# Optimization experiments

Hardware: AMD Instinct MI355X
Metric: run time of the kernel (lower is better)

Reference implementation:

```python
import jax, jax.numpy as jnp
import numpy as np

N = 100000      # nodes
E = 1600000     # edges (avg degree 16)
F_IN = 64       # num_features
HID = 16        # hidden channels (fixed in module)
OUT = 32        # num_classes
K = 2           # kernel_size (dim=1, degree=1 open B-spline -> 2 basis fns)


def setup_inputs() -> dict:
    key = jax.random.key(0)
    ks = jax.random.split(key, 8)
    return {
        "x": jax.random.normal(ks[0], (N, F_IN), jnp.float32),
        "edge_index": jax.random.randint(ks[1], (2, E), 0, N, dtype=jnp.int64),
        "dropout": 0,  # unused in eval mode (F.dropout training=False)
        "edge_attr": jnp.full((E, 1), 0.1, jnp.float32),  # nt([0.1]) broadcast per edge
        "W1": jax.random.normal(ks[2], (K, F_IN, HID), jnp.float32) / np.sqrt(K * F_IN).astype(np.float32),
        "root1": jax.random.normal(ks[3], (F_IN, HID), jnp.float32) / np.sqrt(F_IN).astype(np.float32),
        "bias1": jnp.zeros((HID,), jnp.float32),
        "W2": jax.random.normal(ks[4], (K, HID, OUT), jnp.float32) / np.sqrt(K * HID).astype(np.float32),
        "root2": jax.random.normal(ks[5], (HID, OUT), jnp.float32) / np.sqrt(HID).astype(np.float32),
        "bias2": jnp.zeros((OUT,), jnp.float32),
    }


def spline_conv(x, edge_index, edge_attr, W, root, bias):
    """SplineConv, dim=1, kernel_size=2, degree=1 open B-spline, aggr='mean'."""
    src, dst = edge_index[0], edge_index[1]
    n = x.shape[0]
    u = edge_attr[:, 0]                                  # [E] pseudo-coords in [0,1]
    # degree-1 open spline, kernel_size=2: frac = u*(ks-1) = u; kernels {0,1}
    basis = jnp.stack([1.0 - u, u], axis=1)              # [E, K]
    # transform at node level (cheaper than gathering raw features per edge)
    h = jnp.einsum('nf,kfo->nko', x, W)                  # [N, K, out]
    msg = jnp.einsum('ek,eko->eo', basis, h[src])        # [E, out]
    summed = jax.ops.segment_sum(msg, dst, num_segments=n)
    deg = jax.ops.segment_sum(jnp.ones_like(u), dst, num_segments=n)
    out = summed / jnp.maximum(deg, 1.0)[:, None]        # mean aggregation
    return out + x @ root + bias                          # root weight + bias


def reference(x, edge_index, dropout, edge_attr, W1, root1, bias1, W2, root2, bias2):
    # dropout is a no-op in eval mode
    h = jax.nn.elu(spline_conv(x, edge_index, edge_attr, W1, root1, bias1))
    h = spline_conv(h, edge_index, edge_attr, W2, root2, bias2)
    return jax.nn.log_softmax(h, axis=1)
```

## Files before the change

kernel.cpp:

```cpp
#include <hip/hip_runtime.h>
#include <math.h>

#define NN 100000
#define NE 1600000
#define F_IN 64
#define HID 16
#define OUTF 32
#define BKT_SHIFT 6
#define BKT_NODES 64
#define NBKT 1563
#define SRCM 0x1FFFF
#define CAP_REG 2048
#define CAP_LDS 1184
#define PBLK3 200
#define EPB3 8000
#define CHUNK 2000
#define NCHK 4
#define OVF_MAX 4096

__device__ __forceinline__ unsigned bf16r(float f) {
    unsigned u = __float_as_uint(f);
    return (u + 0x7FFFu + ((u >> 16) & 1u)) >> 16;
}
__device__ __forceinline__ float bfa(unsigned p) { return __uint_as_float(p << 16); }
__device__ __forceinline__ float bfd(unsigned p) { return __uint_as_float(p & 0xFFFF0000u); }
__device__ __forceinline__ float bfh(unsigned short v) { return __uint_as_float(((unsigned)v) << 16); }

__device__ __forceinline__ void acc8(uint4 hv, float u, float* s0, float* s1) {
    unsigned w[4] = {hv.x, hv.y, hv.z, hv.w};
#pragma unroll
    for (int q = 0; q < 4; ++q) {
        float lo = __uint_as_float(w[q] << 16);
        float hi = __uint_as_float(w[q] & 0xFFFF0000u);
        s0[2 * q]     += lo; s1[2 * q]     = fmaf(u, lo, s1[2 * q]);
        s0[2 * q + 1] += hi; s1[2 * q + 1] = fmaf(u, hi, s1[2 * q + 1]);
    }
}
__device__ __forceinline__ void acc4(uint4 ap, float u, float* a) {
    unsigned w[4] = {ap.x, ap.y, ap.z, ap.w};
#pragma unroll
    for (int q = 0; q < 4; ++q)
        a[q] += fmaf(u, bfd(w[q]), bfa(w[q]));
}

__global__ __launch_bounds__(1024) void partF_kernel(const int* __restrict__ ei,
                                                     const float* __restrict__ ea,
                                                     int* __restrict__ gcur,
                                                     int* __restrict__ novf,
                                                     int4* __restrict__ ovf,
                                                     int2* __restrict__ bkt) {
    __shared__ int gpos[NBKT];
    __shared__ int segc[NBKT];
    __shared__ int pw[16];
    __shared__ int2 sbuf[CHUNK];
    int t = threadIdx.x, blk = blockIdx.x;
    for (int i = t; i < NBKT; i += 1024) gpos[i] = 0;
    __syncthreads();
    int beg = blk * EPB3;
    for (int i = t; i < EPB3 / 4; i += 1024) {
        int4 d4 = *(const int4*)(ei + NE + beg + 4 * i);
        atomicAdd(&gpos[d4.x >> BKT_SHIFT], 1);
        atomicAdd(&gpos[d4.y >> BKT_SHIFT], 1);
        atomicAdd(&gpos[d4.z >> BKT_SHIFT], 1);
        atomicAdd(&gpos[d4.w >> BKT_SHIFT], 1);
    }
    __syncthreads();
    int rot = (blk * 397) % NBKT;
    for (int k = t; k < NBKT; k += 1024) {
        int i = k + rot; if (i >= NBKT) i -= NBKT;
        int c = gpos[i];
        gpos[i] = c ? atomicAdd(&gcur[i], c) : 0;
    }
    __syncthreads();
    for (int c = 0; c < NCHK; ++c) {
        int cbeg = beg + c * CHUNK;
        for (int i = t; i < NBKT; i += 1024) segc[i] = 0;
        __syncthreads();
        for (int i = t; i < CHUNK / 4; i += 1024) {
            int4 d4 = *(const int4*)(ei + NE + cbeg + 4 * i);
            atomicAdd(&segc[d4.x >> BKT_SHIFT], 1);
            atomicAdd(&segc[d4.y >> BKT_SHIFT], 1);
            atomicAdd(&segc[d4.z >> BKT_SHIFT], 1);
            atomicAdd(&segc[d4.w >> BKT_SHIFT], 1);
        }
        __syncthreads();
        int i0 = 2 * t, i1 = 2 * t + 1;
        int v0 = (i0 < NBKT) ? segc[i0] : 0;
        int v1 = (i1 < NBKT) ? segc[i1] : 0;
        int ts = v0 + v1;
        int lane = t & 63, wid = t >> 6;
        int sc = ts;
#pragma unroll
        for (int off = 1; off < 64; off <<= 1) {
            int o = __shfl_up(sc, off, 64);
            if (lane >= off) sc += o;
        }
        if (lane == 63) pw[wid] = sc;
        __syncthreads();
        if (t < 16) {
            int p = pw[t];
            int q = p;
#pragma unroll
            for (int off = 1; off < 16; off <<= 1) {
                int o = __shfl_up(q, off, 64);
                if (t >= off) q += o;
            }
            pw[t] = q - p;
        }
        __syncthreads();
        int ebase = pw[wid] + (sc - ts);
        if (i0 < NBKT) segc[i0] = ebase;
        if (i1 < NBKT) segc[i1] = ebase + v0;
        __syncthreads();
        for (int i = t; i < CHUNK / 4; i += 1024) {
            int4 d4 = *(const int4*)(ei + NE + cbeg + 4 * i);
            int4 s4 = *(const int4*)(ei + cbeg + 4 * i);
            float4 u4 = *(const float4*)(ea + cbeg + 4 * i);
            int dst[4] = {d4.x, d4.y, d4.z, d4.w};
            int src[4] = {s4.x, s4.y, s4.z, s4.w};
            float uu[4] = {u4.x, u4.y, u4.z, u4.w};
#pragma unroll
            for (int k = 0; k < 4; ++k) {
                int b = dst[k] >> BKT_SHIFT;
                int pos = atomicAdd(&segc[b], 1);
                sbuf[pos] = make_int2(src[k] | ((dst[k] & (BKT_NODES - 1)) << 17),
                                      __float_as_int(uu[k]));
            }
        }
        __syncthreads();
        for (int i = t; i < CHUNK; i += 1024) {
            int lo = 0, hi = NBKT - 1;
            while (lo < hi) {
                int mid = (lo + hi) >> 1;
                if (segc[mid] > i) hi = mid; else lo = mid + 1;
            }
            int b = lo;
            int start = b ? segc[b - 1] : 0;
            int p = gpos[b] + (i - start);
            int2 pk = sbuf[i];
            if (p < CAP_REG) {
                bkt[(size_t)b * CAP_REG + p] = pk;
            } else {
                int o = atomicAdd(novf, 1);
                if (o < OVF_MAX)
                    ovf[o] = make_int4(b * BKT_NODES + (((unsigned)pk.x) >> 17), pk.x & SRCM, pk.y, 0);
            }
        }
        __syncthreads();
        for (int b = t; b < NBKT; b += 1024) {
            int start = b ? segc[b - 1] : 0;
            gpos[b] += segc[b] - start;
        }
        __syncthreads();
    }
}

__global__ __launch_bounds__(256) void proj1z_kernel(const float* __restrict__ x,
                                                     const float* __restrict__ W1,
                                                     const float* __restrict__ root1,
                                                     const float* __restrict__ bias1,
                                                     unsigned* __restrict__ ab1p,
                                                     float* __restrict__ r1,
                                                     int* __restrict__ gcur,
                                                     int* __restrict__ novf) {
    int gz = blockIdx.x * 256 + threadIdx.x;
    if (gz < NBKT) gcur[gz] = 0;
    if (gz == NBKT) novf[0] = 0;
    __shared__ float w[2 * F_IN * HID];
    __shared__ float wr[F_IN * HID];
    __shared__ float bb[HID];
    for (int i = threadIdx.x; i < 2 * F_IN * HID; i += 256) w[i] = W1[i];
    for (int i = threadIdx.x; i < F_IN * HID; i += 256) wr[i] = root1[i];
    if (threadIdx.x < HID) bb[threadIdx.x] = bias1[threadIdx.x];
    __syncthreads();
    int n = blockIdx.x * 256 + threadIdx.x;
    if (n >= NN) return;
    float accA[HID], accB[HID], accR[HID];
#pragma unroll
    for (int o = 0; o < HID; ++o) { accA[o] = 0.f; accB[o] = 0.f; accR[o] = bb[o]; }
    const float4* xr4 = (const float4*)(x + (size_t)n * F_IN);
    for (int f4 = 0; f4 < F_IN / 4; ++f4) {
        float4 xv4 = xr4[f4];
        float xs[4] = {xv4.x, xv4.y, xv4.z, xv4.w};
#pragma unroll
        for (int q = 0; q < 4; ++q) {
            int f = f4 * 4 + q;
            float xv = xs[q];
            const float* w0 = &w[f * HID];
            const float* w1 = &w[F_IN * HID + f * HID];
            const float* w2 = &wr[f * HID];
#pragma unroll
            for (int o = 0; o < HID; ++o) {
                accA[o] = fmaf(xv, w0[o], accA[o]);
                accB[o] = fmaf(xv, w1[o], accB[o]);
                accR[o] = fmaf(xv, w2[o], accR[o]);
            }
        }
    }
    unsigned* ar = ab1p + (size_t)n * HID;
    float* rr = r1 + (size_t)n * HID;
#pragma unroll
    for (int o = 0; o < HID; ++o) {
        ar[o] = bf16r(accA[o]) | (bf16r(accB[o] - accA[o]) << 16);
        rr[o] = accR[o];
    }
}

__global__ __launch_bounds__(256) void gather1_kernel(const int* __restrict__ gcur,
                                                      const int* __restrict__ novf,
                                                      const int4* __restrict__ ovf,
                                                      int2* __restrict__ bkt,
                                                      const unsigned* __restrict__ ab1p,
                                                      const float* __restrict__ r1,
                                                      unsigned short* __restrict__ h16,
                                                      float* __restrict__ dinv,
                                                      int* __restrict__ segg) {
    __shared__ int2 sorted[CAP_LDS];
    __shared__ int cnt[BKT_NODES], cur[BKT_NODES], segb[BKT_NODES + 1];
    __shared__ float degsL[BKT_NODES];
    int t = threadIdx.x;
    int b = blockIdx.x;
    int tot = gcur[b];
    int beg = b * CAP_REG;
    if (t < BKT_NODES) { cnt[t] = 0; cur[t] = 0; degsL[t] = 0.f; }
    __syncthreads();
    int nodeBase = b * BKT_NODES;

    if (tot <= CAP_LDS) {
        int2 myE[5];
        int nE = 0;
        for (int e = t; e < tot; e += 256) {
            int2 pk = bkt[beg + e];
            myE[nE++] = pk;
            atomicAdd(&cnt[((unsigned)pk.x) >> 17], 1);
        }
        __syncthreads();
        if (t < BKT_NODES) {
            int v = cnt[t];
            int sc = v;
#pragma unroll
            for (int off = 1; off < 64; off <<= 1) {
                int o = __shfl_up(sc, off, 64);
                if (t >= off) sc += o;
            }
            segb[t] = sc - v;
            if (t == 63) segb[64] = sc;
        }
        __syncthreads();
        for (int k = 0; k < nE; ++k) {
            int loc = ((unsigned)myE[k].x) >> 17;
            int pos = segb[loc] + atomicAdd(&cur[loc], 1);
            sorted[pos] = myE[k];
        }
        __syncthreads();
        int nv = tot >> 1;
        int4* s4 = (int4*)sorted;
        int4* o4 = (int4*)(bkt + beg);
        for (int i = t; i < nv; i += 256) o4[i] = s4[i];
        if (t == 0 && (tot & 1)) bkt[beg + tot - 1] = sorted[tot - 1];
        if (t <= BKT_NODES) segg[b * (BKT_NODES + 1) + t] = segb[t];
        int node = t >> 2;
        int jq = t & 3;
        int s0 = segb[node], e2 = segb[node + 1];
        float acc[4] = {0.f, 0.f, 0.f, 0.f};
        int e = s0;
        for (; e + 3 < e2; e += 4) {
            int2 p0 = sorted[e];
            int2 p1 = sorted[e + 1];
            int2 p2 = sorted[e + 2];
            int2 p3 = sorted[e + 3];
            uint4 a0 = *(const uint4*)(ab1p + ((size_t)(p0.x & SRCM) << 4) + (jq << 2));
            uint4 a1 = *(const uint4*)(ab1p + ((size_t)(p1.x & SRCM) << 4) + (jq << 2));
            uint4 a2 = *(const uint4*)(ab1p + ((size_t)(p2.x & SRCM) << 4) + (jq << 2));
            uint4 a3 = *(const uint4*)(ab1p + ((size_t)(p3.x & SRCM) << 4) + (jq << 2));
            acc4(a0, __int_as_float(p0.y), acc);
            acc4(a1, __int_as_float(p1.y), acc);
            acc4(a2, __int_as_float(p2.y), acc);
            acc4(a3, __int_as_float(p3.y), acc);
        }
        for (; e < e2; ++e) {
            int2 pk = sorted[e];
            uint4 ap = *(const uint4*)(ab1p + ((size_t)(pk.x & SRCM) << 4) + (jq << 2));
            acc4(ap, __int_as_float(pk.y), acc);
        }
        int n = nodeBase + node;
        if (n < NN) {
            float d0 = 1.f / (float)max(e2 - s0, 1);
            float4 rv = *(const float4*)(r1 + ((size_t)n << 4) + (jq << 2));
            float rr[4] = {rv.x, rv.y, rv.z, rv.w};
            unsigned hw[4];
#pragma unroll
            for (int k = 0; k < 4; ++k) {
                float v = acc[k] * d0 + rr[k];
                hw[k] = bf16r(v > 0.f ? v : expm1f(v));
            }
            *(uint2*)(h16 + ((size_t)n << 4) + (jq << 2)) =
                make_uint2(hw[0] | (hw[1] << 16), hw[2] | (hw[3] << 16));
            if (jq == 0) dinv[n] = d0;
        }
    } else {
        float* accL = (float*)sorted;
        int inreg = min(tot, CAP_REG);
        int end = beg + inreg;
        for (int i = t; i < BKT_NODES * HID; i += 256) accL[i] = 0.f;
        __syncthreads();
        int j = t & (HID - 1);
        int g = t >> 4;
        for (int e = beg + g; e < end; e += 16) {
            int2 pk = bkt[e];
            unsigned p = ab1p[(size_t)(pk.x & SRCM) * HID + j];
            atomicAdd(&accL[(((unsigned)pk.x) >> 17) * HID + j],
                      fmaf(__int_as_float(pk.y), bfd(p), bfa(p)));
            if (j == 0) atomicAdd(&degsL[((unsigned)pk.x) >> 17], 1.f);
        }
        int ovn = min(novf[0], OVF_MAX);
        for (int o = 0; o < ovn; ++o) {
            int4 ent = ovf[o];
            int loc = ent.x - nodeBase;
            if (loc >= 0 && loc < BKT_NODES && g == 0) {
                unsigned p = ab1p[(size_t)ent.y * HID + j];
                atomicAdd(&accL[loc * HID + j], fmaf(__int_as_float(ent.z), bfd(p), bfa(p)));
                if (j == 0) atomicAdd(&degsL[loc], 1.f);
            }
        }
        __syncthreads();
        if (t < BKT_NODES) degsL[t] = 1.f / fmaxf(degsL[t], 1.f);
        if (t == 0) segg[b * (BKT_NODES + 1)] = -1;
        __syncthreads();
        for (int idx = t; idx < BKT_NODES * HID; idx += 256) {
            int nl = idx >> 4, jj = idx & (HID - 1);
            int n = nodeBase + nl;
            if (n < NN) {
                float v = accL[idx] * degsL[nl] + r1[(size_t)n * HID + jj];
                h16[(size_t)n * HID + jj] = (unsigned short)bf16r(v > 0.f ? v : expm1f(v));
            }
        }
        if (t < BKT_NODES && nodeBase + t < NN) dinv[nodeBase + t] = degsL[t];
    }
}

#define HB_NODES 32
__global__ __launch_bounds__(256) void gather2_kernel(const int* __restrict__ gcur,
                                                      const int* __restrict__ novf,
                                                      const int4* __restrict__ ovf,
                                                      const int2* __restrict__ bkt,
                                                      const unsigned short* __restrict__ h16,
                                                      const float* __restrict__ W2,
                                                      const float* __restrict__ root2,
                                                      const float* __restrict__ bias2,
                                                      const float* __restrict__ dinv,
                                                      const int* __restrict__ segg,
                                                      float* __restrict__ out) {
    __shared__ float w20[HID * OUTF], w2d[HID * OUTF], wr[HID * OUTF];
    __shared__ float bb[OUTF];
    __shared__ int segb[HB_NODES + 1];
    __shared__ int sflag;
    int t = threadIdx.x;
    int b2 = blockIdx.x;
    int b = b2 >> 1;
    int h = b2 & 1;
    for (int i = t; i < HID * OUTF; i += 256) {
        float a = W2[i];
        w20[i] = a;
        w2d[i] = W2[HID * OUTF + i] - a;
        wr[i] = root2[i];
    }
    if (t < OUTF) bb[t] = bias2[t];
    int tot = gcur[b];
    int beg = b * CAP_REG;
    int nodeBase = b * BKT_NODES + h * HB_NODES;
    if (t <= HB_NODES) segb[t] = segg[b * (BKT_NODES + 1) + h * HB_NODES + t];
    if (t == 0) sflag = segg[b * (BKT_NODES + 1)];
    __syncthreads();

    int node = t >> 3;
    int li = t & 7;
    int sub = li >> 1;
    int jh = li & 1;
    float S0[8] = {0.f, 0.f, 0.f, 0.f, 0.f, 0.f, 0.f, 0.f};
    float S1[8] = {0.f, 0.f, 0.f, 0.f, 0.f, 0.f, 0.f, 0.f};

    if (tot <= CAP_LDS && sflag != -1) {
        const int2* sp = bkt + beg;
        int s = segb[node], e2 = segb[node + 1];
        int e = s + sub;
        for (; e + 12 < e2; e += 16) {
            int2 p0 = sp[e];
            int2 p1 = sp[e + 4];
            int2 p2 = sp[e + 8];
            int2 p3 = sp[e + 12];
            uint4 h0 = *(const uint4*)(h16 + ((size_t)(p0.x & SRCM) << 4) + (jh << 3));
            uint4 h1 = *(const uint4*)(h16 + ((size_t)(p1.x & SRCM) << 4) + (jh << 3));
            uint4 h2 = *(const uint4*)(h16 + ((size_t)(p2.x & SRCM) << 4) + (jh << 3));
            uint4 h3 = *(const uint4*)(h16 + ((size_t)(p3.x & SRCM) << 4) + (jh << 3));
            acc8(h0, __int_as_float(p0.y), S0, S1);
            acc8(h1, __int_as_float(p1.y), S0, S1);
            acc8(h2, __int_as_float(p2.y), S0, S1);
            acc8(h3, __int_as_float(p3.y), S0, S1);
        }
        for (; e < e2; e += 4) {
            int2 pk = sp[e];
            uint4 hv = *(const uint4*)(h16 + ((size_t)(pk.x & SRCM) << 4) + (jh << 3));
            acc8(hv, __int_as_float(pk.y), S0, S1);
        }
#pragma unroll
        for (int k = 0; k < 8; ++k) {
            S0[k] += __shfl_xor(S0[k], 2); S0[k] += __shfl_xor(S0[k], 4);
            S1[k] += __shfl_xor(S1[k], 2); S1[k] += __shfl_xor(S1[k], 4);
        }
    } else {
        float* s0L = w20;
        float* s1L = w2d;
        for (int i = t; i < HB_NODES * HID; i += 256) { s0L[i] = 0.f; s1L[i] = 0.f; }
        __syncthreads();
        int j = t & (HID - 1);
        int g = t >> 4;
        int inreg = min(tot, CAP_REG);
        int end = beg + inreg;
        for (int e = beg + g; e < end; e += 16) {
            int2 pk = bkt[e];
            int loc = ((unsigned)pk.x) >> 17;
            if ((loc >> 5) == h) {
                float hvv = bfh(h16[(size_t)(pk.x & SRCM) * HID + j]);
                atomicAdd(&s0L[(loc & 31) * HID + j], hvv);
                atomicAdd(&s1L[(loc & 31) * HID + j], __int_as_float(pk.y) * hvv);
            }
        }
        int ovn = min(novf[0], OVF_MAX);
        for (int o = 0; o < ovn; ++o) {
            int4 ent = ovf[o];
            int loc = ent.x - nodeBase;
            if (loc >= 0 && loc < HB_NODES && g == 0) {
                float hvv = bfh(h16[(size_t)ent.y * HID + j]);
                atomicAdd(&s0L[loc * HID + j], hvv);
                atomicAdd(&s1L[loc * HID + j], __int_as_float(ent.z) * hvv);
            }
        }
        __syncthreads();
#pragma unroll
        for (int k = 0; k < 8; ++k) {
            S0[k] = s0L[node * HID + jh * 8 + k];
            S1[k] = s1L[node * HID + jh * 8 + k];
        }
        __syncthreads();
        for (int i = t; i < HID * OUTF; i += 256) {
            float a = W2[i];
            w20[i] = a;
            w2d[i] = W2[HID * OUTF + i] - a;
        }
        __syncthreads();
    }

    float F0[16], F1[16];
#pragma unroll
    for (int k = 0; k < 8; ++k) {
        float p0 = __shfl_xor(S0[k], 1);
        float p1 = __shfl_xor(S1[k], 1);
        F0[k] = jh ? p0 : S0[k];
        F0[8 + k] = jh ? S0[k] : p0;
        F1[k] = jh ? p1 : S1[k];
        F1[8 + k] = jh ? S1[k] : p1;
    }
    int n = nodeBase + node;
    if (n < NN) {
        float di = dinv[n];
        uint4 hA = *(const uint4*)(h16 + ((size_t)n << 4));
        uint4 hB = *(const uint4*)(h16 + ((size_t)n << 4) + 8);
        float hf[16];
        unsigned wa[4] = {hA.x, hA.y, hA.z, hA.w};
        unsigned wb[4] = {hB.x, hB.y, hB.z, hB.w};
#pragma unroll
        for (int q = 0; q < 4; ++q) {
            hf[2 * q]     = __uint_as_float(wa[q] << 16);
            hf[2 * q + 1] = __uint_as_float(wa[q] & 0xFFFF0000u);
            hf[8 + 2 * q]     = __uint_as_float(wb[q] << 16);
            hf[8 + 2 * q + 1] = __uint_as_float(wb[q] & 0xFFFF0000u);
        }
        float outv[4];
#pragma unroll
        for (int q = 0; q < 4; ++q) {
            int jj = li * 4 + q;
            float ms = 0.f;
#pragma unroll
            for (int f = 0; f < HID; ++f)
                ms += F0[f] * w20[f * OUTF + jj] + F1[f] * w2d[f * OUTF + jj];
            float v = ms * di + bb[jj];
#pragma unroll
            for (int f = 0; f < HID; ++f)
                v = fmaf(hf[f], wr[f * OUTF + jj], v);
            outv[q] = v;
        }
        float m = fmaxf(fmaxf(outv[0], outv[1]), fmaxf(outv[2], outv[3]));
        m = fmaxf(m, __shfl_xor(m, 1));
        m = fmaxf(m, __shfl_xor(m, 2));
        m = fmaxf(m, __shfl_xor(m, 4));
        float sl = expf(outv[0] - m) + expf(outv[1] - m) + expf(outv[2] - m) + expf(outv[3] - m);
        sl += __shfl_xor(sl, 1);
        sl += __shfl_xor(sl, 2);
        sl += __shfl_xor(sl, 4);
        float lse = m + logf(sl);
        *(float4*)(out + (size_t)n * OUTF + li * 4) =
            make_float4(outv[0] - lse, outv[1] - lse, outv[2] - lse, outv[3] - lse);
    }
}

extern "C" void kernel_launch(void* const* d_in, const int* in_sizes, int n_in,
                              void* d_out, int out_size, void* d_ws, size_t ws_size,
                              hipStream_t stream) {
    const float* x     = (const float*)d_in[0];
    const int*   ei    = (const int*)d_in[1];
    const float* ea    = (const float*)d_in[3];
    const float* W1    = (const float*)d_in[4];
    const float* root1 = (const float*)d_in[5];
    const float* bias1 = (const float*)d_in[6];
    const float* W2    = (const float*)d_in[7];
    const float* root2 = (const float*)d_in[8];
    const float* bias2 = (const float*)d_in[9];
    float* out = (float*)d_out;
    float* ws  = (float*)d_ws;

    const size_t N = NN;
    int*            gcur = (int*)(ws);
    int*            novf = (int*)(ws + 2000);
    int4*           ovf  = (int4*)(ws + 2048);
    float*          dinv = ws + 20000;
    int*            segg = (int*)(ws + 120000);
    float*          r1   = ws + 222000;
    unsigned*       ab1p = (unsigned*)(ws + 222000 + 16 * N);
    unsigned short* h16  = (unsigned short*)(ws + 222000 + 32 * N);
    int2*           bkt  = (int2*)(ws + 222000 + 40 * N);

    int nbN = (NN + 255) / 256;
    proj1z_kernel<<<nbN, 256, 0, stream>>>(x, W1, root1, bias1, ab1p, r1, gcur, novf);
    partF_kernel<<<PBLK3, 1024, 0, stream>>>(ei, ea, gcur, novf, ovf, bkt);
    gather1_kernel<<<NBKT, 256, 0, stream>>>(gcur, novf, ovf, bkt, ab1p, r1, h16, dinv, segg);
    gather2_kernel<<<NBKT * 2, 256, 0, stream>>>(gcur, novf, ovf, bkt, h16, W2, root2, bias2, dinv, segg, out);
}
```

Baseline: 111.5 us.

## Run node projection concurrently with edge partitioning in one fused launch

```diff
diff --git a/kernel.cpp b/kernel.cpp
--- a/kernel.cpp
+++ b/kernel.cpp
@@ -17,6 +17,7 @@
 #define CHUNK 2000
 #define NCHK 4
 #define OVF_MAX 4096
+#define PROJ_BLKS 98
 
 __device__ __forceinline__ unsigned bf16r(float f) {
     unsigned u = __float_as_uint(f);
@@ -43,17 +44,73 @@
         a[q] += fmaf(u, bfd(w[q]), bfa(w[q]));
 }
 
-__global__ __launch_bounds__(1024) void partF_kernel(const int* __restrict__ ei,
-                                                     const float* __restrict__ ea,
-                                                     int* __restrict__ gcur,
-                                                     int* __restrict__ novf,
-                                                     int4* __restrict__ ovf,
-                                                     int2* __restrict__ bkt) {
+__global__ __launch_bounds__(256) void zeroG_kernel(int* __restrict__ gcur,
+                                                    int* __restrict__ novf) {
+    int t = blockIdx.x * 256 + threadIdx.x;
+    if (t < NBKT) gcur[t] = 0;
+    if (t == NBKT) novf[0] = 0;
+}
+
+__global__ __launch_bounds__(1024) void fusedPP_kernel(const int* __restrict__ ei,
+                                                       const float* __restrict__ ea,
+                                                       int* __restrict__ gcur,
+                                                       int* __restrict__ novf,
+                                                       int4* __restrict__ ovf,
+                                                       int2* __restrict__ bkt,
+                                                       const float* __restrict__ x,
+                                                       const float* __restrict__ W1,
+                                                       const float* __restrict__ root1,
+                                                       const float* __restrict__ bias1,
+                                                       unsigned* __restrict__ ab1p,
+                                                       float* __restrict__ r1) {
     __shared__ int gpos[NBKT];
     __shared__ int segc[NBKT];
     __shared__ int pw[16];
     __shared__ int2 sbuf[CHUNK];
     int t = threadIdx.x, blk = blockIdx.x;
+
+    if (blk >= PBLK3) {
+        float* w  = (float*)sbuf;
+        float* wr = (float*)gpos;
+        __shared__ float bb[HID];
+        for (int i = t; i < 2 * F_IN * HID; i += 1024) w[i] = W1[i];
+        for (int i = t; i < F_IN * HID; i += 1024) wr[i] = root1[i];
+        if (t < HID) bb[t] = bias1[t];
+        __syncthreads();
+        int n = (blk - PBLK3) * 1024 + t;
+        if (n >= NN) return;
+        float accA[HID], accB[HID], accR[HID];
+#pragma unroll
+        for (int o = 0; o < HID; ++o) { accA[o] = 0.f; accB[o] = 0.f; accR[o] = bb[o]; }
+        const float4* xr4 = (const float4*)(x + (size_t)n * F_IN);
+        for (int f4 = 0; f4 < F_IN / 4; ++f4) {
+            float4 xv4 = xr4[f4];
+            float xs[4] = {xv4.x, xv4.y, xv4.z, xv4.w};
+#pragma unroll
+            for (int q = 0; q < 4; ++q) {
+                int f = f4 * 4 + q;
+                float xv = xs[q];
+                const float* w0 = &w[f * HID];
+                const float* w1 = &w[F_IN * HID + f * HID];
+                const float* w2 = &wr[f * HID];
+#pragma unroll
+                for (int o = 0; o < HID; ++o) {
+                    accA[o] = fmaf(xv, w0[o], accA[o]);
+                    accB[o] = fmaf(xv, w1[o], accB[o]);
+                    accR[o] = fmaf(xv, w2[o], accR[o]);
+                }
+            }
+        }
+        unsigned* ar = ab1p + (size_t)n * HID;
+        float* rr = r1 + (size_t)n * HID;
+#pragma unroll
+        for (int o = 0; o < HID; ++o) {
+            ar[o] = bf16r(accA[o]) | (bf16r(accB[o] - accA[o]) << 16);
+            rr[o] = accR[o];
+        }
+        return;
+    }
+
     for (int i = t; i < NBKT; i += 1024) gpos[i] = 0;
     __syncthreads();
     int beg = blk * EPB3;
@@ -152,57 +209,6 @@
             gpos[b] += segc[b] - start;
         }
         __syncthreads();
-    }
-}
-
-__global__ __launch_bounds__(256) void proj1z_kernel(const float* __restrict__ x,
-                                                     const float* __restrict__ W1,
-                                                     const float* __restrict__ root1,
-                                                     const float* __restrict__ bias1,
-                                                     unsigned* __restrict__ ab1p,
-                                                     float* __restrict__ r1,
-                                                     int* __restrict__ gcur,
-                                                     int* __restrict__ novf) {
-    int gz = blockIdx.x * 256 + threadIdx.x;
-    if (gz < NBKT) gcur[gz] = 0;
-    if (gz == NBKT) novf[0] = 0;
-    __shared__ float w[2 * F_IN * HID];
-    __shared__ float wr[F_IN * HID];
-    __shared__ float bb[HID];
-    for (int i = threadIdx.x; i < 2 * F_IN * HID; i += 256) w[i] = W1[i];
-    for (int i = threadIdx.x; i < F_IN * HID; i += 256) wr[i] = root1[i];
-    if (threadIdx.x < HID) bb[threadIdx.x] = bias1[threadIdx.x];
-    __syncthreads();
-    int n = blockIdx.x * 256 + threadIdx.x;
-    if (n >= NN) return;
-    float accA[HID], accB[HID], accR[HID];
-#pragma unroll
-    for (int o = 0; o < HID; ++o) { accA[o] = 0.f; accB[o] = 0.f; accR[o] = bb[o]; }
-    const float4* xr4 = (const float4*)(x + (size_t)n * F_IN);
-    for (int f4 = 0; f4 < F_IN / 4; ++f4) {
-        float4 xv4 = xr4[f4];
-        float xs[4] = {xv4.x, xv4.y, xv4.z, xv4.w};
-#pragma unroll
-        for (int q = 0; q < 4; ++q) {
-            int f = f4 * 4 + q;
-            float xv = xs[q];
-            const float* w0 = &w[f * HID];
-            const float* w1 = &w[F_IN * HID + f * HID];
-            const float* w2 = &wr[f * HID];
-#pragma unroll
-            for (int o = 0; o < HID; ++o) {
-                accA[o] = fmaf(xv, w0[o], accA[o]);
-                accB[o] = fmaf(xv, w1[o], accB[o]);
-                accR[o] = fmaf(xv, w2[o], accR[o]);
-            }
-        }
-    }
-    unsigned* ar = ab1p + (size_t)n * HID;
-    float* rr = r1 + (size_t)n * HID;
-#pragma unroll
-    for (int o = 0; o < HID; ++o) {
-        ar[o] = bf16r(accA[o]) | (bf16r(accB[o] - accA[o]) << 16);
-        rr[o] = accR[o];
     }
 }
 
@@ -530,9 +536,9 @@
     unsigned short* h16  = (unsigned short*)(ws + 222000 + 32 * N);
     int2*           bkt  = (int2*)(ws + 222000 + 40 * N);
 
-    int nbN = (NN + 255) / 256;
-    proj1z_kernel<<<nbN, 256, 0, stream>>>(x, W1, root1, bias1, ab1p, r1, gcur, novf);
-    partF_kernel<<<PBLK3, 1024, 0, stream>>>(ei, ea, gcur, novf, ovf, bkt);
+    zeroG_kernel<<<(NBKT + 256) / 256, 256, 0, stream>>>(gcur, novf);
+    fusedPP_kernel<<<PBLK3 + PROJ_BLKS, 1024, 0, stream>>>(ei, ea, gcur, novf, ovf, bkt,
+                                                           x, W1, root1, bias1, ab1p, r1);
     gather1_kernel<<<NBKT, 256, 0, stream>>>(gcur, novf, ovf, bkt, ab1p, r1, h16, dinv, segg);
     gather2_kernel<<<NBKT * 2, 256, 0, stream>>>(gcur, novf, ovf, bkt, h16, W2, root2, bias2, dinv, segg, out);
 }
```

Result: slower. 123.2 us (+10.5%).
